# Kernel optimization log

Hardware: AMD Instinct MI355X
Metric: run time of the kernel (lower is better)

Reference implementation:

```python
import jax, jax.numpy as jnp
import numpy as np

DIM = 512
HEADS = 8
HEAD_DIM = DIM // HEADS
SCALE = HEAD_DIM ** -0.5


def setup_inputs() -> dict:
    key = jax.random.key(0)
    k1, k2, k3, k4, k5 = jax.random.split(key, 5)
    x = jax.random.normal(k1, (2, 4096, DIM), dtype=jnp.float32)
    # qkv Linear: weight [3*dim, dim], bias [3*dim]; proj: [dim, dim], [dim]
    w_qkv = jax.random.normal(k2, (3 * DIM, DIM), dtype=jnp.float32) * (DIM ** -0.5)
    b_qkv = jax.random.normal(k3, (3 * DIM,), dtype=jnp.float32) * 0.02
    w_proj = jax.random.normal(k4, (DIM, DIM), dtype=jnp.float32) * (DIM ** -0.5)
    b_proj = jax.random.normal(k5, (DIM,), dtype=jnp.float32) * 0.02
    return {"x": x, "w_qkv": w_qkv, "b_qkv": b_qkv, "w_proj": w_proj, "b_proj": b_proj}


def reference(x, w_qkv, b_qkv, w_proj, b_proj):
    B, N, C = x.shape
    qkv = x @ w_qkv.T + b_qkv  # [B, N, 3C]
    qkv = qkv.reshape(B, N, 3, HEADS, HEAD_DIM).transpose(2, 0, 3, 1, 4)  # [3,B,H,N,hd]
    q, k, v = qkv[0], qkv[1], qkv[2]
    attn = jnp.einsum('bhnd,bhmd->bhnm', q, k) * SCALE  # explicit NxN matrix
    attn = jax.nn.softmax(attn, axis=-1)
    out = jnp.einsum('bhnm,bhmd->bhnd', attn, v)  # [B,H,N,hd]
    out = out.transpose(0, 2, 1, 3).reshape(B, N, C)
    return out @ w_proj.T + b_proj
```

## Files before the change

kernel.cpp:

```cpp
#include <hip/hip_runtime.h>

typedef __bf16 bf16x8 __attribute__((ext_vector_type(8)));
typedef __bf16 bf16x4 __attribute__((ext_vector_type(4)));
typedef __bf16 bf16x2 __attribute__((ext_vector_type(2)));
typedef float  floatx4 __attribute__((ext_vector_type(4)));
typedef unsigned int uint32;
typedef uint32 uintx4 __attribute__((ext_vector_type(4)));

#define MFMA16(a,b,c) __builtin_amdgcn_mfma_f32_16x16x32_bf16(a,b,c,0,0,0)

constexpr int DIM  = 512;
constexpr int SEQ  = 4096;
constexpr int HD   = 64;
constexpr float QSCALE = 0.1803368801111244f;

static __device__ inline __bf16 f2bf(float f) {
    unsigned int u = __builtin_bit_cast(unsigned int, f);
    u += 0x7fffu + ((u >> 16) & 1u);
    return __builtin_bit_cast(__bf16, (unsigned short)(u >> 16));
}
#if __has_builtin(__builtin_amdgcn_cvt_pk_bf16_f32)
static __device__ inline bf16x2 pk2(float a, float b) {
    return __builtin_amdgcn_cvt_pk_bf16_f32(a, b);
}
#else
static __device__ inline bf16x2 pk2(float a, float b) {
    bf16x2 r; r[0] = f2bf(a); r[1] = f2bf(b); return r;
}
#endif
#if __has_builtin(__builtin_amdgcn_exp2f)
#define EXP2(x) __builtin_amdgcn_exp2f(x)
#else
#define EXP2(x) exp2f(x)
#endif
static __device__ inline bf16x8 cvt8(floatx4 lo, floatx4 hi) {
    uintx4 w;
    w[0] = __builtin_bit_cast(uint32, pk2(lo[0], lo[1]));
    w[1] = __builtin_bit_cast(uint32, pk2(lo[2], lo[3]));
    w[2] = __builtin_bit_cast(uint32, pk2(hi[0], hi[1]));
    w[3] = __builtin_bit_cast(uint32, pk2(hi[2], hi[3]));
    return __builtin_bit_cast(bf16x8, w);
}


__global__ __launch_bounds__(256)
void cvt_blk(const float* __restrict__ X, const float* __restrict__ Wq,
             const float* __restrict__ Wp,
             __bf16* __restrict__ Xb, __bf16* __restrict__ Wqb,
             __bf16* __restrict__ Wpb)
{
    const int slice = blockIdx.y;
    const float* src;
    __bf16* dst;
    int n8;
    if (slice == 0)      { src = X;  dst = Xb;  n8 = (2*SEQ*DIM)/8; }
    else if (slice == 1) { src = Wq; dst = Wqb; n8 = (3*DIM*DIM)/8; }
    else                 { src = Wp; dst = Wpb; n8 = (DIM*DIM)/8; }
    const int i = blockIdx.x * 256 + threadIdx.x;
    if (i >= n8) return;
    const int row = i >> 6;
    const int d0  = (i & 63) * 8;
    const floatx4 lo = *(const floatx4*)(src + (size_t)i*8);
    const floatx4 hi = *(const floatx4*)(src + (size_t)i*8 + 4);
    const size_t off8 = ((size_t)(row >> 4)*16 + (d0 >> 5))*64
                        + ((d0 >> 3) & 3)*16 + (row & 15);
    *(bf16x8*)(dst + off8*8) = cvt8(lo, hi);
}

__global__ __launch_bounds__(256)
void gemm_qkv(const __bf16* __restrict__ Xb, const __bf16* __restrict__ Wb,
              const float* __restrict__ bias,
              __bf16* __restrict__ Qb, __bf16* __restrict__ Kb, __bf16* __restrict__ Vb)
{
    const int tid  = threadIdx.x;
    const int lane = tid & 63;
    const int wave = tid >> 6;
    const int quad = lane >> 4;
    const int l16  = lane & 15;
    const int waveM = wave >> 1, waveN = wave & 1;
    const int mBase = blockIdx.x * 128;
    const int nBase = blockIdx.y * 128;
    const int which = nBase >> 9;

    floatx4 zero = {0.f, 0.f, 0.f, 0.f};
    floatx4 acc[4][4];
    for (int i = 0; i < 4; i++)
        for (int j = 0; j < 4; j++) acc[i][j] = zero;

    const __bf16* ga = Xb + (size_t)(mBase + waveM*64)*512 + lane*8;
    const __bf16* gb = Wb + (size_t)(nBase + waveN*64)*512 + lane*8;

    for (int it = 0; it < 16; ++it) {
        bf16x8 af[4], bfr[4];
        for (int mi = 0; mi < 4; mi++)
            af[mi]  = *(const bf16x8*)(ga + mi*8192 + it*512);
        for (int ni = 0; ni < 4; ni++)
            bfr[ni] = *(const bf16x8*)(gb + ni*8192 + it*512);
        if (which == 2) {
            for (int mi = 0; mi < 4; mi++)
                for (int ni = 0; ni < 4; ni++)
                    acc[mi][ni] = MFMA16(af[mi], bfr[ni], acc[mi][ni]);
        } else {
            for (int mi = 0; mi < 4; mi++)
                for (int ni = 0; ni < 4; ni++)
                    acc[mi][ni] = MFMA16(bfr[ni], af[mi], acc[mi][ni]);
        }
    }

    if (which == 2) {
        for (int ni = 0; ni < 4; ni++) {
            const int n = nBase + waveN*64 + ni*16 + l16;
            const float bv = bias[n];
            const int h = (n >> 6) & 7;
            const int d = n & 63;
            for (int mi = 0; mi < 4; mi++) {
                const int m0 = mBase + waveM*64 + mi*16 + quad*4;
                const int b  = m0 >> 12;
                const int s0 = m0 & 4095;
                const int bh = (b << 3) | h;
                bf16x4 v;
                for (int rr = 0; rr < 4; rr++) v[rr] = f2bf(acc[mi][ni][rr] + bv);
                size_t off = (((((size_t)bh*128 + (s0 >> 5))*4 + (d >> 4))*64)
                              + ((s0 >> 2) & 3)*16 + (d & 15))*8 + ((s0 >> 4) & 1)*4;
                *(bf16x4*)&Vb[off] = v;
            }
        }
    } else {
        __bf16* dst = (which == 0) ? Qb : Kb;
        for (int ni = 0; ni < 4; ni++) {
            const int n0 = nBase + waveN*64 + ni*16 + quad*4;
            const floatx4 b4 = *(const floatx4*)&bias[n0];
            const int dfull = n0 & 511;
            const int h  = dfull >> 6;
            const int d0 = dfull & 63;
            const int lgrp = ((d0 >> 3) & 3)*16 + l16;
            const int half = d0 >> 5;
            const int slot = d0 & 7;
            for (int mi = 0; mi < 4; mi++) {
                const int m = mBase + waveM*64 + mi*16 + l16;
                const int b = m >> 12, s = m & 4095;
                const int bh = (b << 3) | h;
                bf16x4 v;
                for (int rr = 0; rr < 4; rr++) {
                    float val = acc[mi][ni][rr] + b4[rr];
                    if (which == 0) val *= QSCALE;
                    v[rr] = f2bf(val);
                }
                size_t off = ((((size_t)bh*256 + (s >> 4))*2 + half)*64 + lgrp)*8 + slot;
                *(bf16x4*)&dst[off] = v;
            }
        }
    }
}

__global__ __launch_bounds__(256, 3)
void attn_kernel(const __bf16* __restrict__ Qb, const __bf16* __restrict__ Kb,
                 const __bf16* __restrict__ Vb, __bf16* __restrict__ Ao)
{
    __shared__ __bf16 Ob[3][64*68];
    __shared__ float  Lb[4][64];
    const int tid  = threadIdx.x;
    const int lane = tid & 63;
    const int wave = tid >> 6;
    const int quad = lane >> 4;
    const int l16  = lane & 15;
    const int id    = blockIdx.x;
    const int slot  = id >> 3;
    const int bh    = (id & 7) + ((slot >> 6) << 3);
    const int qBase = (slot & 63) * 64;

    const __bf16* qg = Qb + (size_t)bh*256*2*512;
    const __bf16* kg = Kb + (size_t)bh*256*2*512;
    const __bf16* vg = Vb + (size_t)bh*128*4*512;

    bf16x8 qf[4][2];
    for (int t = 0; t < 4; t++)
        for (int hb = 0; hb < 2; hb++)
            qf[t][hb] = *(const bf16x8*)(qg
                + ((size_t)((qBase >> 4) + t)*2 + hb)*512 + lane*8);

    floatx4 zero = {0.f, 0.f, 0.f, 0.f};
    floatx4 oacc[4][4];
    for (int t = 0; t < 4; t++)
        for (int od = 0; od < 4; od++) oacc[t][od] = zero;
    floatx4 Lt[4];
    for (int t = 0; t < 4; t++) Lt[t] = zero;

    bf16x8 ones;
    for (int j = 0; j < 8; j++) ones[j] = f2bf(1.0f);

    const int key_begin = wave * 1024;
    const __bf16* kptr = kg + (size_t)(key_begin >> 4)*1024 + lane*8;
    const __bf16* vptr = vg + (size_t)(key_begin >> 5)*2048 + lane*8;

    for (int c = 0; c < 32; ++c) {
        bf16x8 kb00 = *(const bf16x8*)(kptr);
        bf16x8 kb01 = *(const bf16x8*)(kptr + 512);
        bf16x8 kb10 = *(const bf16x8*)(kptr + 1024);
        bf16x8 kb11 = *(const bf16x8*)(kptr + 1536);
        bf16x8 vb0  = *(const bf16x8*)(vptr);
        bf16x8 vb1  = *(const bf16x8*)(vptr + 512);
        bf16x8 vb2  = *(const bf16x8*)(vptr + 1024);
        bf16x8 vb3  = *(const bf16x8*)(vptr + 1536);
        kptr += 2048;
        vptr += 2048;

        for (int t = 0; t < 4; t++) {
            floatx4 z0 = zero, z1 = zero;
            z0 = MFMA16(kb00, qf[t][0], z0);
            z0 = MFMA16(kb01, qf[t][1], z0);
            z1 = MFMA16(kb10, qf[t][0], z1);
            z1 = MFMA16(kb11, qf[t][1], z1);
            float e0[4], e1[4];
            for (int r = 0; r < 4; r++) { e0[r] = EXP2(z0[r]); e1[r] = EXP2(z1[r]); }
            uintx4 w;
            w[0] = __builtin_bit_cast(uint32, pk2(e0[0], e0[1]));
            w[1] = __builtin_bit_cast(uint32, pk2(e0[2], e0[3]));
            w[2] = __builtin_bit_cast(uint32, pk2(e1[0], e1[1]));
            w[3] = __builtin_bit_cast(uint32, pk2(e1[2], e1[3]));
            bf16x8 pb = __builtin_bit_cast(bf16x8, w);
            Lt[t] = MFMA16(ones, pb, Lt[t]);
            oacc[t][0] = MFMA16(vb0, pb, oacc[t][0]);
            oacc[t][1] = MFMA16(vb1, pb, oacc[t][1]);
            oacc[t][2] = MFMA16(vb2, pb, oacc[t][2]);
            oacc[t][3] = MFMA16(vb3, pb, oacc[t][3]);
        }
    }

    if (lane < 16)
        for (int t = 0; t < 4; t++) Lb[wave][t*16 + lane] = Lt[t][0];
    __syncthreads();
    float inv[4];
    for (int t = 0; t < 4; t++) {
        const int q = t*16 + l16;
        inv[t] = 1.0f / (Lb[0][q] + Lb[1][q] + Lb[2][q] + Lb[3][q]);
    }
    if (wave != 0) {
        for (int t = 0; t < 4; t++)
            for (int od = 0; od < 4; od++) {
                bf16x4 v;
                for (int r = 0; r < 4; r++) v[r] = f2bf(oacc[t][od][r] * inv[t]);
                *(bf16x4*)&Ob[wave-1][(t*16 + l16)*68 + od*16 + quad*4] = v;
            }
    }
    __syncthreads();
    if (wave == 0) {
        const int b = bh >> 3, h = bh & 7;
        for (int t = 0; t < 4; t++) {
            const size_t rtop = (size_t)b*256 + (qBase >> 4) + t;
            for (int od = 0; od < 4; od++) {
                bf16x4 o0 = *(const bf16x4*)&Ob[0][(t*16 + l16)*68 + od*16 + quad*4];
                bf16x4 o1 = *(const bf16x4*)&Ob[1][(t*16 + l16)*68 + od*16 + quad*4];
                bf16x4 o2 = *(const bf16x4*)&Ob[2][(t*16 + l16)*68 + od*16 + quad*4];
                bf16x4 v;
                for (int r = 0; r < 4; r++) {
                    float o = oacc[t][od][r] * inv[t] +
                              (float)o0[r] + (float)o1[r] + (float)o2[r];
                    v[r] = f2bf(o);
                }
                const size_t off8 = (rtop*16 + h*2 + (od >> 1))*64
                                    + ((od*2 + (quad >> 1)) & 3)*16 + l16;
                *(bf16x4*)&Ao[off8*8 + (quad & 1)*4] = v;
            }
        }
    }
}

__global__ __launch_bounds__(256)
void gemm_proj(const __bf16* __restrict__ Ab, const __bf16* __restrict__ Wb,
               const float* __restrict__ bias, float* __restrict__ Out)
{
    const int tid  = threadIdx.x;
    const int lane = tid & 63;
    const int wave = tid >> 6;
    const int quad = lane >> 4;
    const int l16  = lane & 15;
    const int waveM = wave >> 1, waveN = wave & 1;
    const int mBase = blockIdx.x * 64;
    const int nBase = blockIdx.y * 64;

    floatx4 zero = {0.f, 0.f, 0.f, 0.f};
    floatx4 acc[2][2];
    for (int i = 0; i < 2; i++)
        for (int j = 0; j < 2; j++) acc[i][j] = zero;

    const __bf16* gA = Ab + (size_t)(mBase + waveM*32)*512 + lane*8;
    const __bf16* gB = Wb + (size_t)(nBase + waveN*32)*512 + lane*8;

    for (int it = 0; it < 16; ++it) {
        bf16x8 af[2], bfr[2];
        for (int mi = 0; mi < 2; mi++)
            af[mi]  = *(const bf16x8*)(gA + mi*8192 + it*512);
        for (int ni = 0; ni < 2; ni++)
            bfr[ni] = *(const bf16x8*)(gB + ni*8192 + it*512);
        for (int mi = 0; mi < 2; mi++)
            for (int ni = 0; ni < 2; ni++)
                acc[mi][ni] = MFMA16(af[mi], bfr[ni], acc[mi][ni]);
    }

    for (int ni = 0; ni < 2; ni++) {
        const int n = nBase + waveN*32 + ni*16 + l16;
        const float bv = bias[n];
        for (int mi = 0; mi < 2; mi++) {
            const int m0 = mBase + waveM*32 + mi*16 + quad*4;
            for (int rr = 0; rr < 4; rr++)
                Out[(size_t)(m0 + rr)*DIM + n] = acc[mi][ni][rr] + bv;
        }
    }
}

extern "C" void kernel_launch(void* const* d_in, const int* in_sizes, int n_in,
                              void* d_out, int out_size, void* d_ws, size_t ws_size,
                              hipStream_t stream) {
    const float* x      = (const float*)d_in[0];
    const float* w_qkv  = (const float*)d_in[1];
    const float* b_qkv  = (const float*)d_in[2];
    const float* w_proj = (const float*)d_in[3];
    const float* b_proj = (const float*)d_in[4];
    float* out = (float*)d_out;

    __bf16* ws  = (__bf16*)d_ws;
    const size_t PLANE = (size_t)16 * SEQ * HD;
    __bf16* Qbk = ws;
    __bf16* Kbk = ws + PLANE;
    __bf16* Vbk = ws + 2*PLANE;
    __bf16* Aob = ws + 3*PLANE;
    __bf16* Xb  = ws + 4*PLANE;
    __bf16* Wqb = ws + 5*PLANE;
    __bf16* Wpb = ws + 5*PLANE + (size_t)3*DIM*DIM;

    cvt_blk<<<dim3(2048, 3), 256, 0, stream>>>(x, w_qkv, w_proj, Xb, Wqb, Wpb);
    gemm_qkv<<<dim3(64, 12), 256, 0, stream>>>(Xb, Wqb, b_qkv, Qbk, Kbk, Vbk);
    attn_kernel<<<dim3(1024), 256, 0, stream>>>(Qbk, Kbk, Vbk, Aob);
    gemm_proj<<<dim3(128, 8), 256, 0, stream>>>(Aob, Wpb, b_proj, out);
}
```

Measured before the change: 184.1 us.

## Double-buffer K tiles in LDS via async global_load_lds prefetch in attention

K fragments are now prefetched one chunk ahead into a per-wave double buffer in LDS using global_load_lds, with explicit vmcnt waits and sched barriers, while V still loads straight to registers. The aim is to hide global-load latency for K behind the MFMA and exp work of the current chunk. The LDS is shared with the output-reduction buffer through a union. This adds LDS traffic and manual waitcnt ordering; there is no barrier between the per-wave LDS write and read, and the fallback path writes LDS synchronously.

```diff
diff --git a/kernel.cpp b/kernel.cpp
--- a/kernel.cpp
+++ b/kernel.cpp
@@ -40,6 +40,16 @@
     w[2] = __builtin_bit_cast(uint32, pk2(hi[0], hi[1]));
     w[3] = __builtin_bit_cast(uint32, pk2(hi[2], hi[3]));
     return __builtin_bit_cast(bf16x8, w);
+}
+
+static __device__ inline void gload16(const __bf16* g, __bf16* l) {
+#if __has_builtin(__builtin_amdgcn_global_load_lds)
+    __builtin_amdgcn_global_load_lds(
+        (const __attribute__((address_space(1))) unsigned int*)g,
+        (__attribute__((address_space(3))) unsigned int*)l, 16, 0, 0);
+#else
+    *(bf16x8*)(l + (threadIdx.x & 63)*8) = *(const bf16x8*)g;
+#endif
 }
 
 
@@ -153,11 +163,16 @@
     }
 }
 
+union AttnSM {
+    __bf16 kbuf[4][2][2048];
+    __bf16 ob[3][64*68];
+};
+
 __global__ __launch_bounds__(256, 3)
 void attn_kernel(const __bf16* __restrict__ Qb, const __bf16* __restrict__ Kb,
                  const __bf16* __restrict__ Vb, __bf16* __restrict__ Ao)
 {
-    __shared__ __bf16 Ob[3][64*68];
+    __shared__ AttnSM sm;
     __shared__ float  Lb[4][64];
     const int tid  = threadIdx.x;
     const int lane = tid & 63;
@@ -193,15 +208,32 @@
     const __bf16* kptr = kg + (size_t)(key_begin >> 4)*1024 + lane*8;
     const __bf16* vptr = vg + (size_t)(key_begin >> 5)*2048 + lane*8;
 
+    {
+        __bf16* nb = &sm.kbuf[wave][0][0];
+        for (int f = 0; f < 4; ++f)
+            gload16(kptr + f*512, nb + f*512);
+    }
+
     for (int c = 0; c < 32; ++c) {
-        bf16x8 kb00 = *(const bf16x8*)(kptr);
-        bf16x8 kb01 = *(const bf16x8*)(kptr + 512);
-        bf16x8 kb10 = *(const bf16x8*)(kptr + 1024);
-        bf16x8 kb11 = *(const bf16x8*)(kptr + 1536);
-        bf16x8 vb0  = *(const bf16x8*)(vptr);
-        bf16x8 vb1  = *(const bf16x8*)(vptr + 512);
-        bf16x8 vb2  = *(const bf16x8*)(vptr + 1024);
-        bf16x8 vb3  = *(const bf16x8*)(vptr + 1536);
+        const int cur = c & 1;
+        bf16x8 vb0 = *(const bf16x8*)(vptr);
+        bf16x8 vb1 = *(const bf16x8*)(vptr + 512);
+        bf16x8 vb2 = *(const bf16x8*)(vptr + 1024);
+        bf16x8 vb3 = *(const bf16x8*)(vptr + 1536);
+        __builtin_amdgcn_sched_barrier(0);
+        if (c < 31) {
+            __bf16* nb = &sm.kbuf[wave][cur ^ 1][0];
+            for (int f = 0; f < 4; ++f)
+                gload16(kptr + 2048 + f*512, nb + f*512);
+        }
+        __builtin_amdgcn_sched_barrier(0);
+        asm volatile("s_waitcnt vmcnt(4)" ::: "memory");
+        __builtin_amdgcn_sched_barrier(0);
+        const __bf16* kc = &sm.kbuf[wave][cur][0];
+        bf16x8 kb00 = *(const bf16x8*)(kc + lane*8);
+        bf16x8 kb01 = *(const bf16x8*)(kc + 512  + lane*8);
+        bf16x8 kb10 = *(const bf16x8*)(kc + 1024 + lane*8);
+        bf16x8 kb11 = *(const bf16x8*)(kc + 1536 + lane*8);
         kptr += 2048;
         vptr += 2048;
 
@@ -240,7 +272,7 @@
             for (int od = 0; od < 4; od++) {
                 bf16x4 v;
                 for (int r = 0; r < 4; r++) v[r] = f2bf(oacc[t][od][r] * inv[t]);
-                *(bf16x4*)&Ob[wave-1][(t*16 + l16)*68 + od*16 + quad*4] = v;
+                *(bf16x4*)&sm.ob[wave-1][(t*16 + l16)*68 + od*16 + quad*4] = v;
             }
     }
     __syncthreads();
@@ -249,9 +281,9 @@
         for (int t = 0; t < 4; t++) {
             const size_t rtop = (size_t)b*256 + (qBase >> 4) + t;
             for (int od = 0; od < 4; od++) {
-                bf16x4 o0 = *(const bf16x4*)&Ob[0][(t*16 + l16)*68 + od*16 + quad*4];
-                bf16x4 o1 = *(const bf16x4*)&Ob[1][(t*16 + l16)*68 + od*16 + quad*4];
-                bf16x4 o2 = *(const bf16x4*)&Ob[2][(t*16 + l16)*68 + od*16 + quad*4];
+                bf16x4 o0 = *(const bf16x4*)&sm.ob[0][(t*16 + l16)*68 + od*16 + quad*4];
+                bf16x4 o1 = *(const bf16x4*)&sm.ob[1][(t*16 + l16)*68 + od*16 + quad*4];
+                bf16x4 o2 = *(const bf16x4*)&sm.ob[2][(t*16 + l16)*68 + od*16 + quad*4];
                 bf16x4 v;
                 for (int r = 0; r < 4; r++) {
                     float o = oacc[t][od][r] * inv[t] +
```

New measurement: 195.9 us. +6.4%, slower.
